# Kernel optimization log

Hardware: AMD Instinct MI355X
Metric: run time of the kernel (lower is better)

Reference implementation:

```python
import jax, jax.numpy as jnp
import numpy as np

T, H, I, E, K = 1024, 1024, 512, 32, 4   # tokens, hidden, moe_inter, n_experts, top_k
G, TG, NS = 8, 4, 2                      # n_group, topk_group, n_shared_experts
C = 2 * T * K // E                       # expert capacity (no-drop headroom)
SCALE = 2.5                              # routed_scaling_factor


def setup_inputs() -> dict:
    key = jax.random.key(0)
    ks = jax.random.split(key, 7)
    s = 0.02
    return dict(
        hidden_states=jax.random.normal(ks[0], (T, H), jnp.float32),
        gate_w=jax.random.normal(ks[1], (E, H), jnp.float32) * s,
        e_bias=jax.random.normal(ks[2], (E,), jnp.float32) * 0.1,
        w_gate_up=jax.random.normal(ks[3], (E, 2 * I, H), jnp.float32) * s,
        w_down=jax.random.normal(ks[4], (E, H, I), jnp.float32) * s,
        w_gate_up_shared=jax.random.normal(ks[5], (2 * I * NS, H), jnp.float32) * s,
        w_down_shared=jax.random.normal(ks[6], (H, I * NS), jnp.float32) * s,
    )


def reference(hidden_states, gate_w, e_bias, w_gate_up, w_down, w_gate_up_shared, w_down_shared):
    x = hidden_states                                   # (T, H)
    # --- gate + sigmoid scoring (noaux_tc) ---
    logits = x @ gate_w.T                               # (T, E)
    scores = jax.nn.sigmoid(logits.astype(jnp.float32))
    sfc = scores + e_bias                               # scores_for_choice
    # --- group-limited top-k: top-2 sum per group, keep topk_group groups ---
    group_scores = jax.lax.top_k(sfc.reshape(T, G, E // G), 2)[0].sum(-1)  # (T, G)
    grp_idx = jax.lax.top_k(group_scores, TG)[1]        # (T, TG)
    gmask = jnp.zeros((T, G), jnp.float32).at[jnp.arange(T)[:, None], grp_idx].set(1.0)
    smask = jnp.repeat(gmask, E // G, axis=1)           # (T, E)
    sfc_m = jnp.where(smask > 0, sfc, 0.0)
    topk_idx = jax.lax.top_k(sfc_m, K)[1]               # (T, K)
    tw = jnp.take_along_axis(scores, topk_idx, axis=1)  # weights from raw scores
    tw = tw / (tw.sum(-1, keepdims=True) + 1e-20)       # norm_topk_prob
    tw = tw * SCALE
    # --- capacity-based dispatch (position within expert via cumsum of one-hot) ---
    e_flat = topk_idx.reshape(-1)                       # (T*K,)
    oh = jax.nn.one_hot(e_flat, E, dtype=jnp.float32)   # (T*K, E)
    pos = jnp.sum((jnp.cumsum(oh, axis=0) - 1.0) * oh, axis=-1).astype(jnp.int32)
    keep = (pos < C).astype(jnp.float32)                # capacity sized to never drop
    pos_c = jnp.clip(pos, 0, C - 1)
    t_flat = jnp.repeat(jnp.arange(T), K)
    combine = jnp.zeros((T, E, C), jnp.float32).at[t_flat, e_flat, pos_c].add(tw.reshape(-1) * keep)
    dispatch = jnp.zeros((T, E, C), jnp.float32).at[t_flat, e_flat, pos_c].add(keep)
    # --- grouped expert MLP (gate_up -> SiluAndMul -> down) ---
    xe = jnp.einsum('tec,th->ech', dispatch, x)         # (E, C, H)
    gu = jnp.einsum('ech,eoh->eco', xe, w_gate_up)      # (E, C, 2I)
    act = jax.nn.silu(gu[..., :I]) * gu[..., I:]
    ye = jnp.einsum('eci,ehi->ech', act, w_down)        # (E, C, H)
    routed = jnp.einsum('tec,ech->th', combine, ye)     # (T, H)
    # --- shared experts MLP on residual ---
    IS = I * NS
    gus = x @ w_gate_up_shared.T                        # (T, 2*IS)
    acts = jax.nn.silu(gus[:, :IS]) * gus[:, IS:]
    shared = acts @ w_down_shared.T                     # (T, H)
    return routed + shared
```

## Files before the change

### kernel.cpp

```cpp
#include <hip/hip_runtime.h>
#include <hip/hip_bf16.h>
#include <math.h>

#define T_TOK 1024
#define H_DIM 1024
#define I_DIM 512
#define E_NUM 32
#define K_TOP 4
#define G_NUM 8
#define TG_NUM 4
#define CAP 256
#define IS_DIM 1024
#define RSCALE 2.5f

#define MAXTILES 36

#define WS_CNT_OFF    0
#define WS_NT_OFF     128
#define WS_TILE_OFF   256
#define WS_EIDX_OFF   4096
#define WS_WN_OFF     20480
#define WS_STOK_OFF   36864
#define WS_SW_OFF     69632
#define WS_ACT_OFF    102400
#define WS_ACTS_OFF   (102400 + (size_t)E_NUM*CAP*I_DIM*2)
#define WS_XB_OFF     (WS_ACTS_OFF + (size_t)T_TOK*IS_DIM*2)

typedef __attribute__((ext_vector_type(8))) short short8v;
typedef __attribute__((ext_vector_type(4))) float f32x4;
typedef __attribute__((ext_vector_type(4))) unsigned uint4v;

__device__ __forceinline__ short f2bf(float f) {
    unsigned u = __float_as_uint(f);
    u += 0x7FFFu + ((u >> 16) & 1u);
    return (short)(u >> 16);
}
__device__ __forceinline__ unsigned pk2bf(float a, float b) {
    unsigned ua = __float_as_uint(a) + 0x8000u;
    unsigned ub = __float_as_uint(b) + 0x8000u;
    return __builtin_amdgcn_perm(ub, ua, 0x07060302);
}
__device__ __forceinline__ uint4v pk8bf(float4 lo, float4 hi) {
    uint4v r; r.x = pk2bf(lo.x, lo.y); r.y = pk2bf(lo.z, lo.w);
    r.z = pk2bf(hi.x, hi.y); r.w = pk2bf(hi.z, hi.w); return r;
}
__device__ __forceinline__ float silu_(float g) { return g / (1.f + expf(-g)); }

#define LDSTRIDE 40

__global__ __launch_bounds__(256) void gate_kernel(
    const float* __restrict__ x, const float* __restrict__ gate_w,
    const float* __restrict__ e_bias,
    int* __restrict__ eidx, float* __restrict__ wnorm, short* __restrict__ xb)
{
    __shared__ float xs[H_DIM];
    __shared__ float logits[E_NUM];
    const int t = blockIdx.x;
    const int tid = threadIdx.x;
    float4 v = ((const float4*)(x + (size_t)t * H_DIM))[tid];
    ((float4*)xs)[tid] = v;
    {
        unsigned* xd = (unsigned*)(xb + (size_t)t * H_DIM) + tid * 2;
        xd[0] = pk2bf(v.x, v.y); xd[1] = pk2bf(v.z, v.w);
    }
    __syncthreads();

    const int e = tid >> 3, sub = tid & 7;
    const float4* gw4 = (const float4*)(gate_w + (size_t)e * H_DIM + sub * 128);
    const float4* xr4 = (const float4*)(xs + sub * 128);
    float p = 0.f;
    #pragma unroll
    for (int h = 0; h < 32; ++h) {
        float4 a = xr4[h], b = gw4[h];
        p += a.x * b.x + a.y * b.y + a.z * b.z + a.w * b.w;
    }
    for (int off = 4; off; off >>= 1) p += __shfl_down(p, off, 8);
    if (sub == 0) logits[e] = p;
    __syncthreads();
    if (tid != 0) return;

    float sc[E_NUM], sfc[E_NUM];
    for (int i = 0; i < E_NUM; ++i) {
        sc[i] = 1.f / (1.f + expf(-logits[i]));
        sfc[i] = sc[i] + e_bias[i];
    }
    float gs[G_NUM];
    for (int g = 0; g < G_NUM; ++g) {
        float m1 = -1e30f, m2 = -1e30f;
        for (int j = 0; j < E_NUM / G_NUM; ++j) {
            float v2 = sfc[g * (E_NUM / G_NUM) + j];
            if (v2 > m1) { m2 = m1; m1 = v2; } else if (v2 > m2) m2 = v2;
        }
        gs[g] = m1 + m2;
    }
    bool gm[G_NUM];
    for (int g = 0; g < G_NUM; ++g) gm[g] = false;
    for (int it = 0; it < TG_NUM; ++it) {
        int best = -1; float bv = -1e30f;
        for (int g = 0; g < G_NUM; ++g) if (!gm[g] && gs[g] > bv) { bv = gs[g]; best = g; }
        gm[best] = true;
    }
    float sm[E_NUM];
    for (int i = 0; i < E_NUM; ++i) sm[i] = gm[i / (E_NUM / G_NUM)] ? sfc[i] : 0.0f;
    int idx[K_TOP]; float w[K_TOP]; float tsum = 0.f;
    for (int it = 0; it < K_TOP; ++it) {
        int best = 0; float bv = -1e30f;
        for (int i = 0; i < E_NUM; ++i) if (sm[i] > bv) { bv = sm[i]; best = i; }
        sm[best] = -1e30f;
        idx[it] = best; w[it] = sc[best]; tsum += w[it];
    }
    float inv = RSCALE / (tsum + 1e-20f);
    const int base = t * K_TOP;
    for (int it = 0; it < K_TOP; ++it) {
        eidx[base + it] = idx[it];
        wnorm[base + it] = w[it] * inv;
    }
}

__global__ __launch_bounds__(256) void assign_kernel(
    const int* __restrict__ eidx, const float* __restrict__ wnorm,
    int* __restrict__ cnt, int* __restrict__ slot_token, float* __restrict__ slot_w,
    int* __restrict__ ntiles, int* __restrict__ tiles)
{
    __shared__ int   se[T_TOK * K_TOP];
    __shared__ float swt[T_TOK * K_TOP];
    __shared__ int   scnt[E_NUM];
    const int tid = threadIdx.x;
    for (int i = tid; i < T_TOK * K_TOP; i += 256) { se[i] = eidx[i]; swt[i] = wnorm[i]; }
    __syncthreads();

    const int e = tid >> 3;
    const int seg = tid & 7;
    const int base = seg * 512;
    int c = 0;
    for (int i = 0; i < 512; ++i) c += (se[base + i] == e);
    int excl = 0, total = 0;
    for (int s = 0; s < 8; ++s) {
        int cs = __shfl(c, s, 8);
        total += cs;
        if (s < seg) excl += cs;
    }
    if (seg == 0) { cnt[e] = total; scnt[e] = total; }
    int pos = excl;
    for (int i = 0; i < 512; ++i) {
        if (se[base + i] == e) {
            if (pos < CAP) {
                slot_token[e * CAP + pos] = (base + i) >> 2;
                slot_w[e * CAP + pos] = swt[base + i];
            }
            ++pos;
        }
    }
    __syncthreads();
    if (tid == 0) {
        int nt = 0;
        for (int t0 = 0; t0 < T_TOK; t0 += 256) {
            tiles[nt * 4] = -1; tiles[nt * 4 + 1] = t0; tiles[nt * 4 + 2] = 256; ++nt;
        }
        for (int ee = 0; ee < E_NUM; ++ee) {
            int n = min(scnt[ee], CAP);
            if (n > 0) { tiles[nt * 4] = ee; tiles[nt * 4 + 1] = 0; tiles[nt * 4 + 2] = n; ++nt; }
        }
        *ntiles = nt;
    }
}


__global__ __launch_bounds__(512, 2) void gu_all_kernel(
    const short* __restrict__ xb, const float* __restrict__ w_gate_up,
    const float* __restrict__ w_gus,
    const int* __restrict__ ntiles, const int* __restrict__ tiles,
    const int* __restrict__ slot_token, const float* __restrict__ slot_w,
    short* __restrict__ act, short* __restrict__ acts)
{
    if ((int)blockIdx.y >= *ntiles) return;
    const int e  = tiles[blockIdx.y * 4];
    const int r0 = tiles[blockIdx.y * 4 + 1];
    const int ne = tiles[blockIdx.y * 4 + 2];
    const bool sh = (e < 0);
    if (!sh && blockIdx.x >= I_DIM / 64) return;
    const int col0 = blockIdx.x * 64;
    const int mchunks = (ne + 63) >> 6;
    const int rows = mchunks << 6;

    __shared__ __align__(16) short As[2][256 * LDSTRIDE];
    __shared__ __align__(16) short Bs[2][128 * LDSTRIDE];
    __shared__ int   toks[256];
    __shared__ float sws[256];

    const int tid = threadIdx.x;
    const int lane = tid & 63, wid = tid >> 6;
    const int wm = wid & 3, wn = wid >> 2;
    const int lr16 = lane & 15, kc = lane >> 4;
    const int sc_ = tid & 3, srow = tid >> 2;

    if (tid < 256) {
        if (sh) { toks[tid] = r0 + tid; sws[tid] = 1.f; }
        else {
            bool v = tid < ne;
            toks[tid] = v ? slot_token[e * CAP + tid] : 0;
            sws[tid]  = v ? slot_w[e * CAP + tid] : 0.f;
        }
    }
    __syncthreads();

    const int IDim = sh ? IS_DIM : I_DIM;
    const float* wbase = sh ? w_gus : (w_gate_up + (size_t)e * (2 * I_DIM) * H_DIM);
    const int wr = ((srow >> 4) & 1) * IDim + col0 + ((srow >> 5) << 4) + (srow & 15);
    const float* bptr = wbase + (size_t)wr * H_DIM + sc_ * 8;
    const bool a0v = srow < rows;
    const bool a1v = (srow + 128) < rows;
    const short* aptr0 = xb + (size_t)toks[srow] * H_DIM + sc_ * 8;
    const short* aptr1 = xb + (size_t)toks[srow + 128] * H_DIM + sc_ * 8;
    const int aoff0 = srow * LDSTRIDE + sc_ * 8;
    const int aoff1 = (srow + 128) * LDSTRIDE + sc_ * 8;
    const int boff  = srow * LDSTRIDE + sc_ * 8;

    f32x4 acc[4][4];
    #pragma unroll
    for (int i = 0; i < 4; ++i)
        #pragma unroll
        for (int j = 0; j < 4; ++j) acc[i][j] = 0.f;

    short8v cA0{}, cA1{};
    if (a0v) cA0 = *(const short8v*)(aptr0);
    if (a1v) cA1 = *(const short8v*)(aptr1);
    float4 cB0 = *(const float4*)(bptr), cB1 = *(const float4*)(bptr + 4);

    int buf = 0;
    for (int k0 = 0; k0 < H_DIM; k0 += 32) {
        short8v nA0{}, nA1{};
        float4 nB0{}, nB1{};
        const int k1 = k0 + 32;
        if (k1 < H_DIM) {
            if (a0v) nA0 = *(const short8v*)(aptr0 + k1);
            if (a1v) nA1 = *(const short8v*)(aptr1 + k1);
            nB0 = *(const float4*)(bptr + k1); nB1 = *(const float4*)(bptr + k1 + 4);
        }
        if (a0v) *(short8v*)&As[buf][aoff0] = cA0;
        if (a1v) *(short8v*)&As[buf][aoff1] = cA1;
        *(uint4v*)&Bs[buf][boff] = pk8bf(cB0, cB1);
        __syncthreads();
        if (wm < mchunks) {
            short8v a_[4], b_[4];
            #pragma unroll
            for (int mt = 0; mt < 4; ++mt)
                a_[mt] = *(const short8v*)&As[buf][(wm * 64 + mt * 16 + lr16) * LDSTRIDE + kc * 8];
            #pragma unroll
            for (int nt = 0; nt < 4; ++nt)
                b_[nt] = *(const short8v*)&Bs[buf][(wn * 64 + nt * 16 + lr16) * LDSTRIDE + kc * 8];
            #pragma unroll
            for (int mt = 0; mt < 4; ++mt)
                #pragma unroll
                for (int nt = 0; nt < 4; ++nt)
                    acc[mt][nt] = __builtin_amdgcn_mfma_f32_16x16x32_bf16(a_[mt], b_[nt], acc[mt][nt], 0, 0, 0);
        }
        buf ^= 1;
        cA0 = nA0; cA1 = nA1; cB0 = nB0; cB1 = nB1;
    }

    if (wm >= mchunks) return;
    #pragma unroll
    for (int mt = 0; mt < 4; ++mt) {
        #pragma unroll
        for (int q = 0; q < 2; ++q) {
            f32x4 g = acc[mt][2 * q], u = acc[mt][2 * q + 1];
            const int colI = col0 + wn * 32 + q * 16 + lr16;
            #pragma unroll
            for (int i = 0; i < 4; ++i) {
                int r = wm * 64 + mt * 16 + kc * 4 + i;
                if (r < ne) {
                    float s = sws[r];
                    short* dst = sh ? (acts + (size_t)(r0 + r) * IS_DIM + colI)
                                    : (act + ((size_t)e * CAP + r) * I_DIM + colI);
                    *dst = f2bf(s * silu_(g[i]) * u[i]);
                }
            }
        }
    }
}

__global__ __launch_bounds__(512, 2) void down_all_kernel(
    const short* __restrict__ act, const short* __restrict__ acts,
    const float* __restrict__ w_down, const float* __restrict__ w_ds,
    const int* __restrict__ ntiles, const int* __restrict__ tiles,
    const int* __restrict__ slot_token, float* __restrict__ out)
{
    if ((int)blockIdx.y >= *ntiles) return;
    const int e  = tiles[blockIdx.y * 4];
    const int r0 = tiles[blockIdx.y * 4 + 1];
    const int ne = tiles[blockIdx.y * 4 + 2];
    const bool sh = (e < 0);
    const int h0 = blockIdx.x * 128;
    const int mchunks = (ne + 63) >> 6;
    const int rows = mchunks << 6;

    __shared__ __align__(16) short As[2][256 * LDSTRIDE];
    __shared__ __align__(16) short Bs[2][128 * LDSTRIDE];
    __shared__ int toks[256];

    const int tid = threadIdx.x;
    const int lane = tid & 63, wid = tid >> 6;
    const int wm = wid & 3, wn = wid >> 2;
    const int lr16 = lane & 15, kc = lane >> 4;
    const int sc_ = tid & 3, srow = tid >> 2;

    if (tid < 256) {
        if (sh) toks[tid] = r0 + tid;
        else    toks[tid] = (tid < ne) ? slot_token[e * CAP + tid] : 0;
    }
    __syncthreads();

    const int Kdim = sh ? IS_DIM : I_DIM;
    const short* abase = sh ? (acts + (size_t)r0 * IS_DIM) : (act + (size_t)e * CAP * I_DIM);
    const float* wbase = sh ? w_ds : (w_down + (size_t)e * H_DIM * I_DIM);
    const float* bptr  = wbase + (size_t)(h0 + srow) * Kdim + sc_ * 8;
    const bool a0v = srow < rows;
    const bool a1v = (srow + 128) < rows;
    const short* aptr0 = abase + (size_t)srow * Kdim + sc_ * 8;
    const short* aptr1 = abase + (size_t)(srow + 128) * Kdim + sc_ * 8;
    const int aoff0 = srow * LDSTRIDE + sc_ * 8;
    const int aoff1 = (srow + 128) * LDSTRIDE + sc_ * 8;
    const int boff  = srow * LDSTRIDE + sc_ * 8;

    f32x4 acc[4][4];
    #pragma unroll
    for (int i = 0; i < 4; ++i)
        #pragma unroll
        for (int j = 0; j < 4; ++j) acc[i][j] = 0.f;

    short8v cA0{}, cA1{};
    if (a0v) cA0 = *(const short8v*)(aptr0);
    if (a1v) cA1 = *(const short8v*)(aptr1);
    float4 cB0 = *(const float4*)(bptr), cB1 = *(const float4*)(bptr + 4);

    int buf = 0;
    for (int k0 = 0; k0 < Kdim; k0 += 32) {
        short8v nA0{}, nA1{};
        float4 nB0{}, nB1{};
        const int k1 = k0 + 32;
        if (k1 < Kdim) {
            if (a0v) nA0 = *(const short8v*)(aptr0 + k1);
            if (a1v) nA1 = *(const short8v*)(aptr1 + k1);
            nB0 = *(const float4*)(bptr + k1); nB1 = *(const float4*)(bptr + k1 + 4);
        }
        if (a0v) *(short8v*)&As[buf][aoff0] = cA0;
        if (a1v) *(short8v*)&As[buf][aoff1] = cA1;
        *(uint4v*)&Bs[buf][boff] = pk8bf(cB0, cB1);
        __syncthreads();
        if (wm < mchunks) {
            short8v a_[4], b_[4];
            #pragma unroll
            for (int mt = 0; mt < 4; ++mt)
                a_[mt] = *(const short8v*)&As[buf][(wm * 64 + mt * 16 + lr16) * LDSTRIDE + kc * 8];
            #pragma unroll
            for (int nt = 0; nt < 4; ++nt)
                b_[nt] = *(const short8v*)&Bs[buf][(wn * 64 + nt * 16 + lr16) * LDSTRIDE + kc * 8];
            #pragma unroll
            for (int mt = 0; mt < 4; ++mt)
                #pragma unroll
                for (int nt = 0; nt < 4; ++nt)
                    acc[mt][nt] = __builtin_amdgcn_mfma_f32_16x16x32_bf16(a_[mt], b_[nt], acc[mt][nt], 0, 0, 0);
        }
        buf ^= 1;
        cA0 = nA0; cA1 = nA1; cB0 = nB0; cB1 = nB1;
    }

    if (wm >= mchunks) return;
    #pragma unroll
    for (int mt = 0; mt < 4; ++mt) {
        #pragma unroll
        for (int i = 0; i < 4; ++i) {
            int r = wm * 64 + mt * 16 + kc * 4 + i;
            if (r < ne) {
                float* orow = out + (size_t)toks[r] * H_DIM + h0 + wn * 64;
                #pragma unroll
                for (int nt = 0; nt < 4; ++nt)
                    atomicAdd(&orow[nt * 16 + lr16], acc[mt][nt][i]);
            }
        }
    }
}

extern "C" void kernel_launch(void* const* d_in, const int* in_sizes, int n_in,
                              void* d_out, int out_size, void* d_ws, size_t ws_size,
                              hipStream_t stream) {
    const float* x   = (const float*)d_in[0];
    const float* gw  = (const float*)d_in[1];
    const float* eb  = (const float*)d_in[2];
    const float* wgu = (const float*)d_in[3];
    const float* wd  = (const float*)d_in[4];
    const float* wgs = (const float*)d_in[5];
    const float* wds = (const float*)d_in[6];
    float* out = (float*)d_out;
    char* ws = (char*)d_ws;

    int*   cnt    = (int*)(ws + WS_CNT_OFF);
    int*   ntiles = (int*)(ws + WS_NT_OFF);
    int*   tiles  = (int*)(ws + WS_TILE_OFF);
    int*   eidx   = (int*)(ws + WS_EIDX_OFF);
    float* wnorm  = (float*)(ws + WS_WN_OFF);
    int*   stok   = (int*)(ws + WS_STOK_OFF);
    float* sw     = (float*)(ws + WS_SW_OFF);
    short* act    = (short*)(ws + WS_ACT_OFF);
    short* acts   = (short*)(ws + WS_ACTS_OFF);
    short* xb     = (short*)(ws + WS_XB_OFF);

    hipMemsetAsync(out, 0, (size_t)T_TOK * H_DIM * sizeof(float), stream);
    gate_kernel<<<T_TOK, 256, 0, stream>>>(x, gw, eb, eidx, wnorm, xb);
    assign_kernel<<<1, 256, 0, stream>>>(eidx, wnorm, cnt, stok, sw, ntiles, tiles);
    gu_all_kernel<<<dim3(IS_DIM / 64, MAXTILES), 512, 0, stream>>>(
        xb, wgu, wgs, ntiles, tiles, stok, sw, act, acts);
    down_all_kernel<<<dim3(H_DIM / 128, MAXTILES), 512, 0, stream>>>(
        act, acts, wd, wds, ntiles, tiles, stok, out);
}
```

Measured before the change: 437.7 us.

## Drop LDS staging in MoE GEMMs; load MFMA operands directly from global

Both grouped GEMM kernels stop staging A and B tiles through shared memory with per-step barriers. Each wave now loads its MFMA fragments straight from global memory into registers, using a two-stage register double buffer. Blocks shrink to 256 threads with narrower N tiles (32 gate/up columns, 64 hidden columns), which doubles the grid and gives each wave its own B columns. This removes LDS traffic and syncs, but loses cross-wave operand sharing, so each weight and activation element is fetched from global/L2 by more waves.

```diff
diff --git a/kernel.cpp b/kernel.cpp
--- a/kernel.cpp
+++ b/kernel.cpp
@@ -40,13 +40,13 @@
     unsigned ub = __float_as_uint(b) + 0x8000u;
     return __builtin_amdgcn_perm(ub, ua, 0x07060302);
 }
-__device__ __forceinline__ uint4v pk8bf(float4 lo, float4 hi) {
-    uint4v r; r.x = pk2bf(lo.x, lo.y); r.y = pk2bf(lo.z, lo.w);
-    r.z = pk2bf(hi.x, hi.y); r.w = pk2bf(hi.z, hi.w); return r;
+__device__ __forceinline__ short8v cvt8(float4 lo, float4 hi) {
+    union { uint4v u; short8v s; } c;
+    c.u.x = pk2bf(lo.x, lo.y); c.u.y = pk2bf(lo.z, lo.w);
+    c.u.z = pk2bf(hi.x, hi.y); c.u.w = pk2bf(hi.z, hi.w);
+    return c.s;
 }
 __device__ __forceinline__ float silu_(float g) { return g / (1.f + expf(-g)); }
-
-#define LDSTRIDE 40
 
 __global__ __launch_bounds__(256) void gate_kernel(
     const float* __restrict__ x, const float* __restrict__ gate_w,
@@ -166,7 +166,25 @@
 }
 
 
-__global__ __launch_bounds__(512, 2) void gu_all_kernel(
+#define GLOADS_F(B0, B1, AA, KOFF) do { \
+    _Pragma("unroll") for (int nt_ = 0; nt_ < 4; ++nt_) { \
+        B0[nt_] = *(const float4*)(bp[nt_] + (KOFF)); \
+        B1[nt_] = *(const float4*)(bp[nt_] + (KOFF) + 4); } \
+    _Pragma("unroll") for (int mt_ = 0; mt_ < 4; ++mt_) \
+        AA[mt_] = *(const short8v*)(ap[mt_] + (KOFF)); \
+} while (0)
+
+#define GSTEP(B0, B1, AA, KNXT, KLIM) do { \
+    short8v bb_[4], at_[4]; \
+    _Pragma("unroll") for (int nt_ = 0; nt_ < 4; ++nt_) bb_[nt_] = cvt8(B0[nt_], B1[nt_]); \
+    _Pragma("unroll") for (int mt_ = 0; mt_ < 4; ++mt_) at_[mt_] = AA[mt_]; \
+    if ((KNXT) < (KLIM)) GLOADS_F(B0, B1, AA, (KNXT)); \
+    _Pragma("unroll") for (int mt_ = 0; mt_ < 4; ++mt_) \
+    _Pragma("unroll") for (int nt_ = 0; nt_ < 4; ++nt_) \
+        acc[mt_][nt_] = __builtin_amdgcn_mfma_f32_16x16x32_bf16(at_[mt_], bb_[nt_], acc[mt_][nt_], 0, 0, 0); \
+} while (0)
+
+__global__ __launch_bounds__(256, 2) void gu_all_kernel(
     const short* __restrict__ xb, const float* __restrict__ w_gate_up,
     const float* __restrict__ w_gus,
     const int* __restrict__ ntiles, const int* __restrict__ tiles,
@@ -178,43 +196,41 @@
     const int r0 = tiles[blockIdx.y * 4 + 1];
     const int ne = tiles[blockIdx.y * 4 + 2];
     const bool sh = (e < 0);
-    if (!sh && blockIdx.x >= I_DIM / 64) return;
-    const int col0 = blockIdx.x * 64;
+    const int nx = sh ? (IS_DIM / 32) : (I_DIM / 32);
+    if ((int)blockIdx.x >= nx) return;
+    const int col0 = blockIdx.x * 32;
     const int mchunks = (ne + 63) >> 6;
-    const int rows = mchunks << 6;
-
-    __shared__ __align__(16) short As[2][256 * LDSTRIDE];
-    __shared__ __align__(16) short Bs[2][128 * LDSTRIDE];
+
     __shared__ int   toks[256];
     __shared__ float sws[256];
-
     const int tid = threadIdx.x;
-    const int lane = tid & 63, wid = tid >> 6;
-    const int wm = wid & 3, wn = wid >> 2;
-    const int lr16 = lane & 15, kc = lane >> 4;
-    const int sc_ = tid & 3, srow = tid >> 2;
-
-    if (tid < 256) {
-        if (sh) { toks[tid] = r0 + tid; sws[tid] = 1.f; }
-        else {
-            bool v = tid < ne;
-            toks[tid] = v ? slot_token[e * CAP + tid] : 0;
-            sws[tid]  = v ? slot_w[e * CAP + tid] : 0.f;
-        }
-    }
-    __syncthreads();
+    if (sh) { toks[tid] = r0 + tid; sws[tid] = 1.f; }
+    else {
+        bool v = tid < ne;
+        toks[tid] = v ? slot_token[e * CAP + tid] : 0;
+        sws[tid]  = v ? slot_w[e * CAP + tid] : 0.f;
+    }
+    __syncthreads();
+    const int wm = tid >> 6;
+    if (wm >= mchunks) return;
+    const int lane = tid & 63, lr16 = lane & 15, kc = lane >> 4;
 
     const int IDim = sh ? IS_DIM : I_DIM;
     const float* wbase = sh ? w_gus : (w_gate_up + (size_t)e * (2 * I_DIM) * H_DIM);
-    const int wr = ((srow >> 4) & 1) * IDim + col0 + ((srow >> 5) << 4) + (srow & 15);
-    const float* bptr = wbase + (size_t)wr * H_DIM + sc_ * 8;
-    const bool a0v = srow < rows;
-    const bool a1v = (srow + 128) < rows;
-    const short* aptr0 = xb + (size_t)toks[srow] * H_DIM + sc_ * 8;
-    const short* aptr1 = xb + (size_t)toks[srow + 128] * H_DIM + sc_ * 8;
-    const int aoff0 = srow * LDSTRIDE + sc_ * 8;
-    const int aoff1 = (srow + 128) * LDSTRIDE + sc_ * 8;
-    const int boff  = srow * LDSTRIDE + sc_ * 8;
+
+    const float* bp[4];
+    #pragma unroll
+    for (int nt = 0; nt < 4; ++nt) {
+        int r = nt * 16 + lr16;
+        int wr = ((r >> 4) & 1) * IDim + col0 + ((r >> 5) << 4) + (r & 15);
+        bp[nt] = wbase + (size_t)wr * H_DIM + kc * 8;
+    }
+    const short* ap[4];
+    #pragma unroll
+    for (int mt = 0; mt < 4; ++mt) {
+        int r = wm * 64 + mt * 16 + lr16;
+        ap[mt] = xb + (size_t)toks[r] * H_DIM + kc * 8;
+    }
 
     f32x4 acc[4][4];
     #pragma unroll
@@ -222,50 +238,21 @@
         #pragma unroll
         for (int j = 0; j < 4; ++j) acc[i][j] = 0.f;
 
-    short8v cA0{}, cA1{};
-    if (a0v) cA0 = *(const short8v*)(aptr0);
-    if (a1v) cA1 = *(const short8v*)(aptr1);
-    float4 cB0 = *(const float4*)(bptr), cB1 = *(const float4*)(bptr + 4);
-
-    int buf = 0;
-    for (int k0 = 0; k0 < H_DIM; k0 += 32) {
-        short8v nA0{}, nA1{};
-        float4 nB0{}, nB1{};
-        const int k1 = k0 + 32;
-        if (k1 < H_DIM) {
-            if (a0v) nA0 = *(const short8v*)(aptr0 + k1);
-            if (a1v) nA1 = *(const short8v*)(aptr1 + k1);
-            nB0 = *(const float4*)(bptr + k1); nB1 = *(const float4*)(bptr + k1 + 4);
-        }
-        if (a0v) *(short8v*)&As[buf][aoff0] = cA0;
-        if (a1v) *(short8v*)&As[buf][aoff1] = cA1;
-        *(uint4v*)&Bs[buf][boff] = pk8bf(cB0, cB1);
-        __syncthreads();
-        if (wm < mchunks) {
-            short8v a_[4], b_[4];
-            #pragma unroll
-            for (int mt = 0; mt < 4; ++mt)
-                a_[mt] = *(const short8v*)&As[buf][(wm * 64 + mt * 16 + lr16) * LDSTRIDE + kc * 8];
-            #pragma unroll
-            for (int nt = 0; nt < 4; ++nt)
-                b_[nt] = *(const short8v*)&Bs[buf][(wn * 64 + nt * 16 + lr16) * LDSTRIDE + kc * 8];
-            #pragma unroll
-            for (int mt = 0; mt < 4; ++mt)
-                #pragma unroll
-                for (int nt = 0; nt < 4; ++nt)
-                    acc[mt][nt] = __builtin_amdgcn_mfma_f32_16x16x32_bf16(a_[mt], b_[nt], acc[mt][nt], 0, 0, 0);
-        }
-        buf ^= 1;
-        cA0 = nA0; cA1 = nA1; cB0 = nB0; cB1 = nB1;
-    }
-
-    if (wm >= mchunks) return;
+    float4 bA0[4], bA1[4], bB0[4], bB1[4];
+    short8v aA[4], aB[4];
+    GLOADS_F(bA0, bA1, aA, 0);
+    GLOADS_F(bB0, bB1, aB, 32);
+    for (int k0 = 0; k0 < H_DIM; k0 += 64) {
+        GSTEP(bA0, bA1, aA, k0 + 64, H_DIM);
+        GSTEP(bB0, bB1, aB, k0 + 96, H_DIM);
+    }
+
     #pragma unroll
     for (int mt = 0; mt < 4; ++mt) {
         #pragma unroll
         for (int q = 0; q < 2; ++q) {
             f32x4 g = acc[mt][2 * q], u = acc[mt][2 * q + 1];
-            const int colI = col0 + wn * 32 + q * 16 + lr16;
+            const int colI = col0 + q * 16 + lr16;
             #pragma unroll
             for (int i = 0; i < 4; ++i) {
                 int r = wm * 64 + mt * 16 + kc * 4 + i;
@@ -280,7 +267,7 @@
     }
 }
 
-__global__ __launch_bounds__(512, 2) void down_all_kernel(
+__global__ __launch_bounds__(256, 2) void down_all_kernel(
     const short* __restrict__ act, const short* __restrict__ acts,
     const float* __restrict__ w_down, const float* __restrict__ w_ds,
     const int* __restrict__ ntiles, const int* __restrict__ tiles,
@@ -291,37 +278,32 @@
     const int r0 = tiles[blockIdx.y * 4 + 1];
     const int ne = tiles[blockIdx.y * 4 + 2];
     const bool sh = (e < 0);
-    const int h0 = blockIdx.x * 128;
+    const int h0 = blockIdx.x * 64;
     const int mchunks = (ne + 63) >> 6;
-    const int rows = mchunks << 6;
-
-    __shared__ __align__(16) short As[2][256 * LDSTRIDE];
-    __shared__ __align__(16) short Bs[2][128 * LDSTRIDE];
+
     __shared__ int toks[256];
-
     const int tid = threadIdx.x;
-    const int lane = tid & 63, wid = tid >> 6;
-    const int wm = wid & 3, wn = wid >> 2;
-    const int lr16 = lane & 15, kc = lane >> 4;
-    const int sc_ = tid & 3, srow = tid >> 2;
-
-    if (tid < 256) {
-        if (sh) toks[tid] = r0 + tid;
-        else    toks[tid] = (tid < ne) ? slot_token[e * CAP + tid] : 0;
-    }
-    __syncthreads();
+    if (sh) toks[tid] = r0 + tid;
+    else    toks[tid] = (tid < ne) ? slot_token[e * CAP + tid] : 0;
+    __syncthreads();
+    const int wm = tid >> 6;
+    if (wm >= mchunks) return;
+    const int lane = tid & 63, lr16 = lane & 15, kc = lane >> 4;
 
     const int Kdim = sh ? IS_DIM : I_DIM;
     const short* abase = sh ? (acts + (size_t)r0 * IS_DIM) : (act + (size_t)e * CAP * I_DIM);
     const float* wbase = sh ? w_ds : (w_down + (size_t)e * H_DIM * I_DIM);
-    const float* bptr  = wbase + (size_t)(h0 + srow) * Kdim + sc_ * 8;
-    const bool a0v = srow < rows;
-    const bool a1v = (srow + 128) < rows;
-    const short* aptr0 = abase + (size_t)srow * Kdim + sc_ * 8;
-    const short* aptr1 = abase + (size_t)(srow + 128) * Kdim + sc_ * 8;
-    const int aoff0 = srow * LDSTRIDE + sc_ * 8;
-    const int aoff1 = (srow + 128) * LDSTRIDE + sc_ * 8;
-    const int boff  = srow * LDSTRIDE + sc_ * 8;
+
+    const float* bp[4];
+    #pragma unroll
+    for (int nt = 0; nt < 4; ++nt)
+        bp[nt] = wbase + (size_t)(h0 + nt * 16 + lr16) * Kdim + kc * 8;
+    const short* ap[4];
+    #pragma unroll
+    for (int mt = 0; mt < 4; ++mt) {
+        int r = wm * 64 + mt * 16 + lr16;
+        ap[mt] = abase + (size_t)r * Kdim + kc * 8;
+    }
 
     f32x4 acc[4][4];
     #pragma unroll
@@ -329,51 +311,22 @@
         #pragma unroll
         for (int j = 0; j < 4; ++j) acc[i][j] = 0.f;
 
-    short8v cA0{}, cA1{};
-    if (a0v) cA0 = *(const short8v*)(aptr0);
-    if (a1v) cA1 = *(const short8v*)(aptr1);
-    float4 cB0 = *(const float4*)(bptr), cB1 = *(const float4*)(bptr + 4);
-
-    int buf = 0;
-    for (int k0 = 0; k0 < Kdim; k0 += 32) {
-        short8v nA0{}, nA1{};
-        float4 nB0{}, nB1{};
-        const int k1 = k0 + 32;
-        if (k1 < Kdim) {
-            if (a0v) nA0 = *(const short8v*)(aptr0 + k1);
-            if (a1v) nA1 = *(const short8v*)(aptr1 + k1);
-            nB0 = *(const float4*)(bptr + k1); nB1 = *(const float4*)(bptr + k1 + 4);
-        }
-        if (a0v) *(short8v*)&As[buf][aoff0] = cA0;
-        if (a1v) *(short8v*)&As[buf][aoff1] = cA1;
-        *(uint4v*)&Bs[buf][boff] = pk8bf(cB0, cB1);
-        __syncthreads();
-        if (wm < mchunks) {
-            short8v a_[4], b_[4];
-            #pragma unroll
-            for (int mt = 0; mt < 4; ++mt)
-                a_[mt] = *(const short8v*)&As[buf][(wm * 64 + mt * 16 + lr16) * LDSTRIDE + kc * 8];
-            #pragma unroll
-            for (int nt = 0; nt < 4; ++nt)
-                b_[nt] = *(const short8v*)&Bs[buf][(wn * 64 + nt * 16 + lr16) * LDSTRIDE + kc * 8];
-            #pragma unroll
-            for (int mt = 0; mt < 4; ++mt)
-                #pragma unroll
-                for (int nt = 0; nt < 4; ++nt)
-                    acc[mt][nt] = __builtin_amdgcn_mfma_f32_16x16x32_bf16(a_[mt], b_[nt], acc[mt][nt], 0, 0, 0);
-        }
-        buf ^= 1;
-        cA0 = nA0; cA1 = nA1; cB0 = nB0; cB1 = nB1;
-    }
-
-    if (wm >= mchunks) return;
+    float4 bA0[4], bA1[4], bB0[4], bB1[4];
+    short8v aA[4], aB[4];
+    GLOADS_F(bA0, bA1, aA, 0);
+    GLOADS_F(bB0, bB1, aB, 32);
+    for (int k0 = 0; k0 < Kdim; k0 += 64) {
+        GSTEP(bA0, bA1, aA, k0 + 64, Kdim);
+        GSTEP(bB0, bB1, aB, k0 + 96, Kdim);
+    }
+
     #pragma unroll
     for (int mt = 0; mt < 4; ++mt) {
         #pragma unroll
         for (int i = 0; i < 4; ++i) {
             int r = wm * 64 + mt * 16 + kc * 4 + i;
             if (r < ne) {
-                float* orow = out + (size_t)toks[r] * H_DIM + h0 + wn * 64;
+                float* orow = out + (size_t)toks[r] * H_DIM + h0;
                 #pragma unroll
                 for (int nt = 0; nt < 4; ++nt)
                     atomicAdd(&orow[nt * 16 + lr16], acc[mt][nt][i]);
@@ -409,8 +362,8 @@
     hipMemsetAsync(out, 0, (size_t)T_TOK * H_DIM * sizeof(float), stream);
     gate_kernel<<<T_TOK, 256, 0, stream>>>(x, gw, eb, eidx, wnorm, xb);
     assign_kernel<<<1, 256, 0, stream>>>(eidx, wnorm, cnt, stok, sw, ntiles, tiles);
-    gu_all_kernel<<<dim3(IS_DIM / 64, MAXTILES), 512, 0, stream>>>(
+    gu_all_kernel<<<dim3(IS_DIM / 32, MAXTILES), 256, 0, stream>>>(
         xb, wgu, wgs, ntiles, tiles, stok, sw, act, acts);
-    down_all_kernel<<<dim3(H_DIM / 128, MAXTILES), 512, 0, stream>>>(
+    down_all_kernel<<<dim3(H_DIM / 64, MAXTILES), 256, 0, stream>>>(
         act, acts, wd, wds, ntiles, tiles, stok, out);
 }
```

Result: slower. 521.3 us (+19.1%).

## Replace atomic scatter-add in down projection with per-slot buffer plus combine pass

Applied to the files above, without the earlier changes.

The down-projection kernel now writes routed expert outputs with plain stores into a compact per-slot buffer, and shared-expert outputs straight into the output, so it no longer needs atomics or a memset. The assign kernel records a token-to-slot map and per-tile base offsets. A new combine kernel then sums each token's K routed rows into the output. This removes atomic contention and the output memset, at the cost of an extra kernel launch and an extra pass over the routed results.

```diff
diff --git a/kernel.cpp b/kernel.cpp
--- a/kernel.cpp
+++ b/kernel.cpp
@@ -25,6 +25,8 @@
 #define WS_ACT_OFF    102400
 #define WS_ACTS_OFF   (102400 + (size_t)E_NUM*CAP*I_DIM*2)
 #define WS_XB_OFF     (WS_ACTS_OFF + (size_t)T_TOK*IS_DIM*2)
+#define WS_T2S_OFF    (WS_XB_OFF + (size_t)T_TOK*H_DIM*2)
+#define WS_YR_OFF     (WS_T2S_OFF + (size_t)T_TOK*K_TOP*4)
 
 typedef __attribute__((ext_vector_type(8))) short short8v;
 typedef __attribute__((ext_vector_type(4))) float f32x4;
@@ -120,7 +122,7 @@
 __global__ __launch_bounds__(256) void assign_kernel(
     const int* __restrict__ eidx, const float* __restrict__ wnorm,
     int* __restrict__ cnt, int* __restrict__ slot_token, float* __restrict__ slot_w,
-    int* __restrict__ ntiles, int* __restrict__ tiles)
+    int* __restrict__ ntiles, int* __restrict__ tiles, int* __restrict__ tok2slot)
 {
     __shared__ int   se[T_TOK * K_TOP];
     __shared__ float swt[T_TOK * K_TOP];
@@ -141,12 +143,20 @@
         if (s < seg) excl += cs;
     }
     if (seg == 0) { cnt[e] = total; scnt[e] = total; }
+    __syncthreads();
+    int boff = 0;
+    for (int ee = 0; ee < e; ++ee) boff += min(scnt[ee], CAP);
+
     int pos = excl;
     for (int i = 0; i < 512; ++i) {
         if (se[base + i] == e) {
+            const int g = base + i;
             if (pos < CAP) {
-                slot_token[e * CAP + pos] = (base + i) >> 2;
-                slot_w[e * CAP + pos] = swt[base + i];
+                slot_token[e * CAP + pos] = g >> 2;
+                slot_w[e * CAP + pos] = swt[g];
+                tok2slot[g] = boff + pos;
+            } else {
+                tok2slot[g] = -1;
             }
             ++pos;
         }
@@ -155,11 +165,17 @@
     if (tid == 0) {
         int nt = 0;
         for (int t0 = 0; t0 < T_TOK; t0 += 256) {
-            tiles[nt * 4] = -1; tiles[nt * 4 + 1] = t0; tiles[nt * 4 + 2] = 256; ++nt;
-        }
+            tiles[nt * 4] = -1; tiles[nt * 4 + 1] = t0; tiles[nt * 4 + 2] = 256;
+            tiles[nt * 4 + 3] = 0; ++nt;
+        }
+        int off = 0;
         for (int ee = 0; ee < E_NUM; ++ee) {
             int n = min(scnt[ee], CAP);
-            if (n > 0) { tiles[nt * 4] = ee; tiles[nt * 4 + 1] = 0; tiles[nt * 4 + 2] = n; ++nt; }
+            if (n > 0) {
+                tiles[nt * 4] = ee; tiles[nt * 4 + 1] = 0; tiles[nt * 4 + 2] = n;
+                tiles[nt * 4 + 3] = off; ++nt;
+            }
+            off += n;
         }
         *ntiles = nt;
     }
@@ -284,12 +300,13 @@
     const short* __restrict__ act, const short* __restrict__ acts,
     const float* __restrict__ w_down, const float* __restrict__ w_ds,
     const int* __restrict__ ntiles, const int* __restrict__ tiles,
-    const int* __restrict__ slot_token, float* __restrict__ out)
+    float* __restrict__ yr, float* __restrict__ out)
 {
     if ((int)blockIdx.y >= *ntiles) return;
     const int e  = tiles[blockIdx.y * 4];
     const int r0 = tiles[blockIdx.y * 4 + 1];
     const int ne = tiles[blockIdx.y * 4 + 2];
+    const int bo = tiles[blockIdx.y * 4 + 3];
     const bool sh = (e < 0);
     const int h0 = blockIdx.x * 128;
     const int mchunks = (ne + 63) >> 6;
@@ -297,19 +314,12 @@
 
     __shared__ __align__(16) short As[2][256 * LDSTRIDE];
     __shared__ __align__(16) short Bs[2][128 * LDSTRIDE];
-    __shared__ int toks[256];
 
     const int tid = threadIdx.x;
     const int lane = tid & 63, wid = tid >> 6;
     const int wm = wid & 3, wn = wid >> 2;
     const int lr16 = lane & 15, kc = lane >> 4;
     const int sc_ = tid & 3, srow = tid >> 2;
-
-    if (tid < 256) {
-        if (sh) toks[tid] = r0 + tid;
-        else    toks[tid] = (tid < ne) ? slot_token[e * CAP + tid] : 0;
-    }
-    __syncthreads();
 
     const int Kdim = sh ? IS_DIM : I_DIM;
     const short* abase = sh ? (acts + (size_t)r0 * IS_DIM) : (act + (size_t)e * CAP * I_DIM);
@@ -373,13 +383,31 @@
         for (int i = 0; i < 4; ++i) {
             int r = wm * 64 + mt * 16 + kc * 4 + i;
             if (r < ne) {
-                float* orow = out + (size_t)toks[r] * H_DIM + h0 + wn * 64;
+                float* orow = sh ? (out + (size_t)(r0 + r) * H_DIM + h0 + wn * 64)
+                                 : (yr + (size_t)(bo + r) * H_DIM + h0 + wn * 64);
                 #pragma unroll
                 for (int nt = 0; nt < 4; ++nt)
-                    atomicAdd(&orow[nt * 16 + lr16], acc[mt][nt][i]);
+                    orow[nt * 16 + lr16] = acc[mt][nt][i];
             }
         }
     }
+}
+
+__global__ __launch_bounds__(256) void combine_kernel(
+    const float* __restrict__ yr, const int* __restrict__ tok2slot,
+    float* __restrict__ out)
+{
+    const int t = blockIdx.x, tid = threadIdx.x;
+    float4 a = ((const float4*)(out + (size_t)t * H_DIM))[tid];
+    #pragma unroll
+    for (int k = 0; k < K_TOP; ++k) {
+        int s = tok2slot[t * K_TOP + k];
+        if (s >= 0) {
+            float4 b = ((const float4*)(yr + (size_t)s * H_DIM))[tid];
+            a.x += b.x; a.y += b.y; a.z += b.z; a.w += b.w;
+        }
+    }
+    ((float4*)(out + (size_t)t * H_DIM))[tid] = a;
 }
 
 extern "C" void kernel_launch(void* const* d_in, const int* in_sizes, int n_in,
@@ -405,12 +433,14 @@
     short* act    = (short*)(ws + WS_ACT_OFF);
     short* acts   = (short*)(ws + WS_ACTS_OFF);
     short* xb     = (short*)(ws + WS_XB_OFF);
-
-    hipMemsetAsync(out, 0, (size_t)T_TOK * H_DIM * sizeof(float), stream);
+    int*   t2s    = (int*)(ws + WS_T2S_OFF);
+    float* yr     = (float*)(ws + WS_YR_OFF);
+
     gate_kernel<<<T_TOK, 256, 0, stream>>>(x, gw, eb, eidx, wnorm, xb);
-    assign_kernel<<<1, 256, 0, stream>>>(eidx, wnorm, cnt, stok, sw, ntiles, tiles);
+    assign_kernel<<<1, 256, 0, stream>>>(eidx, wnorm, cnt, stok, sw, ntiles, tiles, t2s);
     gu_all_kernel<<<dim3(IS_DIM / 64, MAXTILES), 512, 0, stream>>>(
         xb, wgu, wgs, ntiles, tiles, stok, sw, act, acts);
     down_all_kernel<<<dim3(H_DIM / 128, MAXTILES), 512, 0, stream>>>(
-        act, acts, wd, wds, ntiles, tiles, stok, out);
-}
+        act, acts, wd, wds, ntiles, tiles, yr, out);
+    combine_kernel<<<T_TOK, 256, 0, stream>>>(yr, t2s, out);
+}
```

Result: no change. 439.3 us (+0.4%).
